# Kernel tuning notes

Measured on AMD Instinct MI355X. Metric: run time of the kernel, lower is better.

## Reference

```python
import jax, jax.numpy as jnp
import numpy as np

EPS = 1e-8


def setup_inputs() -> dict:
    key = jax.random.key(0)
    k1, k2, k3, k4 = jax.random.split(key, 4)
    N, Cin, Cout, S, DHW, K = 4, 64, 64, 512, 48, 3
    return {
        "x": jax.random.normal(k1, (N, Cin, DHW, DHW, DHW), dtype=jnp.float32),
        "s": jax.random.normal(k2, (N, S), dtype=jnp.float32),
        "style_weight": jax.random.normal(k3, (Cin, S), dtype=jnp.float32) * (1.0 / np.sqrt(S)),
        "style_bias": jnp.ones((Cin,), dtype=jnp.float32),
        "weight": jax.random.normal(k4, (Cout, Cin, K, K, K), dtype=jnp.float32) * (1.0 / np.sqrt(Cin * K**3)),
        "bias": jnp.zeros((Cout,), dtype=jnp.float32),
    }


def reference(x, s, style_weight, style_bias, weight, bias):
    N, Cin = x.shape[0], x.shape[1]
    Cout = weight.shape[0]
    # style modulation: per-sample per-input-channel scale
    style = s @ style_weight.T + style_bias                      # [N, Cin]
    w = weight[None] * style[:, None, :, None, None, None]       # [N, Cout, Cin, k, k, k]
    # demodulation over fan-in dims (Cin, k, k, k)
    w = w * jax.lax.rsqrt(jnp.sum(w * w, axis=(2, 3, 4, 5), keepdims=True) + EPS)
    w = w.reshape(N * Cout, Cin, *w.shape[3:])                   # grouped kernel
    xg = x.reshape(1, N * Cin, *x.shape[2:])
    y = jax.lax.conv_general_dilated(
        xg, w,
        window_strides=(1, 1, 1),
        padding='VALID',
        feature_group_count=N,
        dimension_numbers=('NCDHW', 'OIDHW', 'NCDHW'),
    )                                                            # [1, N*Cout, D', H', W']
    y = y.reshape(N, Cout, *y.shape[2:])
    return y + bias[None, :, None, None, None]
```

## Files before the change

kernel.cpp:

```cpp
#include <hip/hip_runtime.h>

typedef float f32x4 __attribute__((ext_vector_type(4)));
typedef short bf16x8 __attribute__((ext_vector_type(8)));

#define AS1 __attribute__((address_space(1)))
#define AS3 __attribute__((address_space(3)))

__device__ __forceinline__ void gl16(const void* g, void* l) {
  __builtin_amdgcn_global_load_lds((const AS1 unsigned int*)g,
                                   (AS3 unsigned int*)l, 16, 0, 0);
}

__device__ __forceinline__ unsigned short f2bf(float f) {
  unsigned u = __float_as_uint(f);
  u = u + 0x7FFFu + ((u >> 16) & 1u);
  return (unsigned short)(u >> 16);
}

__global__ __launch_bounds__(256) void k_wmod(const float* __restrict__ s,
                                              const float* __restrict__ sw,
                                              const float* __restrict__ sb,
                                              const float* __restrict__ weight,
                                              unsigned short* __restrict__ wm) {
  int o = blockIdx.x, n = blockIdx.y, t = threadIdx.x;
  int lane = t & 63, wv = t >> 6;
  __shared__ float st4[64][5];
  __shared__ float st[64];
  {
    int i = t >> 2, part = t & 3;
    const float4* swp = (const float4*)(sw + i * 512 + part * 128);
    const float4* sp4 = (const float4*)(s + n * 512 + part * 128);
    float a = 0.f;
#pragma unroll 8
    for (int kk = 0; kk < 32; ++kk) {
      float4 w4 = swp[kk], s4 = sp4[kk];
      a += w4.x * s4.x + w4.y * s4.y + w4.z * s4.z + w4.w * s4.w;
    }
    st4[i][part] = a;
  }
  __syncthreads();
  if (t < 64) st[t] = st4[t][0] + st4[t][1] + st4[t][2] + st4[t][3] + sb[t];
  __syncthreads();

  const float* wp = weight + o * 1728;
  float v[7];
  float ss = 0.f;
#pragma unroll
  for (int j = 0; j < 7; ++j) {
    int idx = t + j * 256;
    float w = 0.f;
    if (idx < 1728) {
      int i = idx / 27;
      w = wp[idx] * st[i];
    }
    v[j] = w;
    ss += w * w;
  }
#pragma unroll
  for (int off = 32; off > 0; off >>= 1) ss += __shfl_down(ss, off);
  __shared__ float red[4];
  if (lane == 0) red[wv] = ss;
  __syncthreads();
  float total = red[0] + red[1] + red[2] + red[3];
  float dm = 1.0f / sqrtf(total + 1e-8f);
#pragma unroll
  for (int j = 0; j < 7; ++j) {
    int idx = t + j * 256;
    if (idx < 1728) {
      int i = idx / 27, k = idx - i * 27;
      int g = (n * 27 + k) * 64 + o;
      wm[g * 64 + (((i >> 3) ^ (o & 7)) << 3) + (i & 7)] = f2bf(v[j] * dm);
    }
  }
}

__global__ __launch_bounds__(256) void k_xpose(const float* __restrict__ x,
                                               unsigned short* __restrict__ xT) {
  __shared__ unsigned tile[256][33];
  int n = blockIdx.y;
  int p0 = blockIdx.x * 256;
  int t = threadIdx.x;
  int wv = t >> 6, lane = t & 63;
  const float* xb = x + (size_t)n * 64 * 110592 + p0 + 4 * lane;
#pragma unroll
  for (int c = 0; c < 8; ++c) {
    int i2 = wv + 4 * c;
    const float4 a = *(const float4*)(xb + (size_t)(2 * i2) * 110592);
    const float4 b = *(const float4*)(xb + (size_t)(2 * i2 + 1) * 110592);
    tile[4 * lane + 0][i2] = (unsigned)f2bf(a.x) | ((unsigned)f2bf(b.x) << 16);
    tile[4 * lane + 1][i2] = (unsigned)f2bf(a.y) | ((unsigned)f2bf(b.y) << 16);
    tile[4 * lane + 2][i2] = (unsigned)f2bf(a.z) | ((unsigned)f2bf(b.z) << 16);
    tile[4 * lane + 3][i2] = (unsigned)f2bf(a.w) | ((unsigned)f2bf(b.w) << 16);
  }
  __syncthreads();
  uint4* dst = (uint4*)xT;
  int sl = t & 7;
#pragma unroll
  for (int pass = 0; pass < 8; ++pass) {
    int p = (t >> 3) + 32 * pass;
    int c = sl ^ (p & 7);
    uint4 u;
    u.x = tile[p][4 * c + 0];
    u.y = tile[p][4 * c + 1];
    u.z = tile[p][4 * c + 2];
    u.w = tile[p][4 * c + 3];
    dst[(size_t)(n * 110592 + p0 + p) * 8 + sl] = u;
  }
}

__global__ __launch_bounds__(256) void k_conv(const unsigned short* __restrict__ xT,
                                              const unsigned short* __restrict__ wm,
                                              const float* __restrict__ bias,
                                              float* __restrict__ out) {
  __shared__ uint4 Bl4[37888 / 16];
  char* Bl = (char*)Bl4;

  int bid = blockIdx.x;
  int orig = (bid & 7) * 276 + (bid >> 3);
  int n = orig / 552;
  int pb = orig - n * 552;
  int p0 = pb * 192;

  int t = threadIdx.x;
  int lane = t & 63, wv = t >> 6;
  int l15 = lane & 15, lhi = lane >> 4;
  f32x4 acc[4][3] = {};

  const char* xb = (const char*)xT + ((size_t)(n * 110592 + p0)) * 128;
  const char* wb = (const char*)wm + (size_t)n * 27 * 8192;

  int aoff[8];
#pragma unroll
  for (int m = 0; m < 4; ++m)
#pragma unroll
    for (int ih = 0; ih < 2; ++ih) {
      int orow = m * 16 + l15;
      int c = lhi + ih * 4;
      aoff[m * 2 + ih] = orow * 128 + ((c ^ (orow & 7)) << 4);
    }

  bf16x8 aA[4], aB[4];
#pragma unroll
  for (int m = 0; m < 4; ++m) aA[m] = *(const bf16x8*)(wb + aoff[m * 2]);

#define STEP(CUR, NXT, U, TP, IHS)                                             \
  do {                                                                         \
    if ((U) + 1 < 54) {                                                        \
      const int u1_ = (U) + 1;                                                 \
      const char* ap_ = wb + (size_t)(u1_ >> 1) * 8192;                        \
      const int ih2_ = u1_ & 1;                                                \
      _Pragma("unroll") for (int m = 0; m < 4; ++m)                            \
          NXT[m] = *(const bf16x8*)(ap_ + aoff[m * 2 + ih2_]);                 \
    }                                                                          \
    __builtin_amdgcn_sched_barrier(0);                                         \
    const int kh_ = (TP) / 3, kw_ = (TP) % 3;                                  \
    const int rb_ = wv * 48 + kh_ * 48 + kw_;                                  \
    const int c_ = lhi + (IHS) * 4;                                            \
    bf16x8 b_[3];                                                              \
    _Pragma("unroll") for (int q = 0; q < 3; ++q) {                            \
      int r_ = rb_ + q * 16 + l15;                                             \
      b_[q] = *(const bf16x8*)(Bl + r_ * 128 + ((c_ ^ (r_ & 7)) << 4));        \
    }                                                                          \
    __builtin_amdgcn_s_setprio(1);                                             \
    _Pragma("unroll") for (int m = 0; m < 4; ++m)                              \
        _Pragma("unroll") for (int q = 0; q < 3; ++q)                          \
            acc[m][q] = __builtin_amdgcn_mfma_f32_16x16x32_bf16(               \
                CUR[m], b_[q], acc[m][q], 0, 0, 0);                            \
    __builtin_amdgcn_s_setprio(0);                                             \
  } while (0)

#pragma unroll
  for (int kd = 0; kd < 3; ++kd) {
    if (kd) __builtin_amdgcn_s_barrier();
    const char* src = xb + (size_t)kd * (2304 * 128);
    for (int cc = wv; cc < 37; cc += 4)
      gl16(src + cc * 1024 + lane * 16, Bl + cc * 1024);
    asm volatile("s_waitcnt vmcnt(0)" ::: "memory");
    __builtin_amdgcn_s_barrier();
    __builtin_amdgcn_sched_barrier(0);
#pragma unroll
    for (int tp = 0; tp < 9; ++tp) {
#pragma unroll
      for (int ihs = 0; ihs < 2; ++ihs) {
        const int u = (kd * 9 + tp) * 2 + ihs;
        if ((u & 1) == 0) STEP(aA, aB, u, tp, ihs);
        else              STEP(aB, aA, u, tp, ihs);
      }
    }
  }
#undef STEP

  float bv[4][4];
#pragma unroll
  for (int m = 0; m < 4; ++m)
#pragma unroll
    for (int r = 0; r < 4; ++r) bv[m][r] = bias[m * 16 + lhi * 4 + r];

  float* ob = out + (size_t)n * 64 * 97336;
#pragma unroll
  for (int q = 0; q < 3; ++q) {
    int p = p0 + wv * 48 + q * 16 + l15;
    int d = p / 2304;
    int rem = p - d * 2304;
    int h = rem / 48;
    int w = rem - h * 48;
    if (h < 46 && w < 46) {
      int base = d * 2116 + h * 46 + w;
#pragma unroll
      for (int m = 0; m < 4; ++m)
#pragma unroll
        for (int r = 0; r < 4; ++r) {
          int o = m * 16 + lhi * 4 + r;
          ob[(size_t)o * 97336 + base] = acc[m][q][r] + bv[m][r];
        }
    }
  }
}

extern "C" void kernel_launch(void* const* d_in, const int* in_sizes, int n_in,
                              void* d_out, int out_size, void* d_ws, size_t ws_size,
                              hipStream_t stream) {
  const float* x    = (const float*)d_in[0];
  const float* s    = (const float*)d_in[1];
  const float* sw   = (const float*)d_in[2];
  const float* sb   = (const float*)d_in[3];
  const float* wt   = (const float*)d_in[4];
  const float* bias = (const float*)d_in[5];
  float* out = (float*)d_out;

  unsigned short* wm    = (unsigned short*)((char*)d_ws + 1024);
  unsigned short* xT    = (unsigned short*)((char*)d_ws + 1024 + 884736);

  hipLaunchKernelGGL(k_wmod, dim3(64, 4), dim3(256), 0, stream, s, sw, sb, wt, wm);
  hipLaunchKernelGGL(k_xpose, dim3(432, 4), dim3(256), 0, stream, x, xT);
  hipLaunchKernelGGL(k_conv, dim3(2208), dim3(256), 0, stream, xT, wm, bias, out);
}
```

Measured before the change: 148.8 us.

## Stage modulated weights through double-buffered LDS via async global-to-LDS loads

Each tap's 8 KB modulated-weight tile was loaded straight from global memory into registers with a one-step register prefetch. Now it is copied into a double-buffered LDS region with global_load_lds while the MFMAs for the current tap run, and A fragments are read from LDS. This removes redundant per-wave global weight loads, but adds a vmcnt wait plus a block barrier after every tap (27 per block) and 16 KB more LDS, which may lower occupancy.

```diff
diff --git a/kernel.cpp b/kernel.cpp
--- a/kernel.cpp
+++ b/kernel.cpp
@@ -113,6 +113,7 @@
                                               const float* __restrict__ bias,
                                               float* __restrict__ out) {
   __shared__ uint4 Bl4[37888 / 16];
+  __shared__ uint4 Al4[2][8192 / 16];
   char* Bl = (char*)Bl4;
 
   int bid = blockIdx.x;
@@ -139,56 +140,57 @@
       aoff[m * 2 + ih] = orow * 128 + ((c ^ (orow & 7)) << 4);
     }
 
-  bf16x8 aA[4], aB[4];
-#pragma unroll
-  for (int m = 0; m < 4; ++m) aA[m] = *(const bf16x8*)(wb + aoff[m * 2]);
-
-#define STEP(CUR, NXT, U, TP, IHS)                                             \
-  do {                                                                         \
-    if ((U) + 1 < 54) {                                                        \
-      const int u1_ = (U) + 1;                                                 \
-      const char* ap_ = wb + (size_t)(u1_ >> 1) * 8192;                        \
-      const int ih2_ = u1_ & 1;                                                \
-      _Pragma("unroll") for (int m = 0; m < 4; ++m)                            \
-          NXT[m] = *(const bf16x8*)(ap_ + aoff[m * 2 + ih2_]);                 \
-    }                                                                          \
-    __builtin_amdgcn_sched_barrier(0);                                         \
-    const int kh_ = (TP) / 3, kw_ = (TP) % 3;                                  \
-    const int rb_ = wv * 48 + kh_ * 48 + kw_;                                  \
-    const int c_ = lhi + (IHS) * 4;                                            \
-    bf16x8 b_[3];                                                              \
-    _Pragma("unroll") for (int q = 0; q < 3; ++q) {                            \
-      int r_ = rb_ + q * 16 + l15;                                             \
-      b_[q] = *(const bf16x8*)(Bl + r_ * 128 + ((c_ ^ (r_ & 7)) << 4));        \
-    }                                                                          \
-    __builtin_amdgcn_s_setprio(1);                                             \
-    _Pragma("unroll") for (int m = 0; m < 4; ++m)                              \
-        _Pragma("unroll") for (int q = 0; q < 3; ++q)                          \
-            acc[m][q] = __builtin_amdgcn_mfma_f32_16x16x32_bf16(               \
-                CUR[m], b_[q], acc[m][q], 0, 0, 0);                            \
-    __builtin_amdgcn_s_setprio(0);                                             \
-  } while (0)
+  {
+    gl16(wb + wv * 1024 + lane * 16, (char*)Al4[0] + wv * 1024);
+    gl16(wb + (wv + 4) * 1024 + lane * 16, (char*)Al4[0] + (wv + 4) * 1024);
+  }
 
 #pragma unroll
   for (int kd = 0; kd < 3; ++kd) {
-    if (kd) __builtin_amdgcn_s_barrier();
     const char* src = xb + (size_t)kd * (2304 * 128);
     for (int cc = wv; cc < 37; cc += 4)
       gl16(src + cc * 1024 + lane * 16, Bl + cc * 1024);
     asm volatile("s_waitcnt vmcnt(0)" ::: "memory");
     __builtin_amdgcn_s_barrier();
     __builtin_amdgcn_sched_barrier(0);
-#pragma unroll
-    for (int tp = 0; tp < 9; ++tp) {
-#pragma unroll
-      for (int ihs = 0; ihs < 2; ++ihs) {
-        const int u = (kd * 9 + tp) * 2 + ihs;
-        if ((u & 1) == 0) STEP(aA, aB, u, tp, ihs);
-        else              STEP(aB, aA, u, tp, ihs);
+
+#pragma unroll
+    for (int tap = 0; tap < 9; ++tap) {
+      const int s = kd * 9 + tap;
+      const int cur = s & 1;
+      if (s + 1 < 27) {
+        const char* ap = wb + (size_t)(s + 1) * 8192;
+        gl16(ap + wv * 1024 + lane * 16, (char*)Al4[cur ^ 1] + wv * 1024);
+        gl16(ap + (wv + 4) * 1024 + lane * 16, (char*)Al4[cur ^ 1] + (wv + 4) * 1024);
       }
-    }
-  }
-#undef STEP
+      const int kh = tap / 3, kw = tap - kh * 3;
+      const int rbase = wv * 48 + kh * 48 + kw;
+      const char* Alc = (const char*)Al4[cur];
+#pragma unroll
+      for (int ih = 0; ih < 2; ++ih) {
+        int c = lhi + ih * 4;
+        bf16x8 a[4], b[3];
+#pragma unroll
+        for (int m = 0; m < 4; ++m)
+          a[m] = *(const bf16x8*)(Alc + aoff[m * 2 + ih]);
+#pragma unroll
+        for (int q = 0; q < 3; ++q) {
+          int r = rbase + q * 16 + l15;
+          b[q] = *(const bf16x8*)(Bl + r * 128 + ((c ^ (r & 7)) << 4));
+        }
+        __builtin_amdgcn_s_setprio(1);
+#pragma unroll
+        for (int m = 0; m < 4; ++m)
+#pragma unroll
+          for (int q = 0; q < 3; ++q)
+            acc[m][q] = __builtin_amdgcn_mfma_f32_16x16x32_bf16(a[m], b[q], acc[m][q], 0, 0, 0);
+        __builtin_amdgcn_s_setprio(0);
+      }
+      asm volatile("s_waitcnt vmcnt(0)" ::: "memory");
+      __builtin_amdgcn_s_barrier();
+      __builtin_amdgcn_sched_barrier(0);
+    }
+  }
 
   float bv[4][4];
 #pragma unroll
```

Result: no change. 151.1 us (+1.6%).
